# Performance work log

Measured on AMD Instinct MI355X. Metric: run time of the kernel, lower is better.

Reference implementation:

```python
import jax, jax.numpy as jnp
import numpy as np


def setup_inputs() -> dict:
    key = jax.random.key(0)
    ks = jax.random.split(key, 24)
    N, C, D_IN, HID, EMB = 8192, 4096, 32, 128, 128
    s = 0.05
    inp = {
        "cand_feat": jax.random.normal(ks[0], (1, C, D_IN), jnp.float32),
        "graph_pos": jax.random.uniform(ks[1], (N, 3), jnp.float32),
        "graph_rad": jax.random.uniform(ks[2], (N,), jnp.float32) + 0.01,
        "L": jnp.ones((1,), jnp.float32),
        "adj": jax.random.uniform(ks[3], (N, N), jnp.float32),
        "mask": jax.random.randint(ks[4], (1, C), 0, 2, jnp.int32),
        # candidate encoder: 32 -> 128 -> 128
        "cW1": jax.random.normal(ks[5], (D_IN, 128), jnp.float32) * s,
        "cb1": jnp.zeros((128,), jnp.float32),
        "cW2": jax.random.normal(ks[6], (128, EMB), jnp.float32) * s,
        "cb2": jnp.zeros((EMB,), jnp.float32),
        # graph encoder input proj: 4 -> 128
        "gW0": jax.random.normal(ks[7], (4, HID), jnp.float32) * s,
        "gb0": jnp.zeros((HID,), jnp.float32),
        # 3 GNN layers: concat(2*HID) -> HID
        "gnnW": jax.random.normal(ks[8], (3, 2 * HID, HID), jnp.float32) * s,
        "gnnb": jnp.zeros((3, HID), jnp.float32),
        # output proj: 2*HID -> EMB
        "goW": jax.random.normal(ks[9], (2 * HID, EMB), jnp.float32) * s,
        "gob": jnp.zeros((EMB,), jnp.float32),
        # fusion: 2*EMB -> 256 -> 128 -> 1
        "fW1": jax.random.normal(ks[10], (2 * EMB, 256), jnp.float32) * s,
        "fb1": jnp.zeros((256,), jnp.float32),
        "fW2": jax.random.normal(ks[11], (256, 128), jnp.float32) * s,
        "fb2": jnp.zeros((128,), jnp.float32),
        "fW3": jax.random.normal(ks[12], (128, 1), jnp.float32) * s,
        "fb3": jnp.zeros((1,), jnp.float32),
    }
    return inp


def reference(cand_feat, graph_pos, graph_rad, L, adj, mask,
              cW1, cb1, cW2, cb2, gW0, gb0, gnnW, gnnb, goW, gob,
              fW1, fb1, fW2, fb2, fW3, fb3):
    relu = jax.nn.relu
    # ---- candidate encoder: [1, C, 32] -> [1, C, 128]
    cand_emb = relu(relu(cand_feat @ cW1 + cb1) @ cW2 + cb2)
    # ---- graph encoder ----
    node = jnp.concatenate([graph_pos / L, (graph_rad / jnp.max(graph_rad))[:, None]], axis=1)  # [N, 4]
    h = relu(node @ gW0 + gb0)  # [N, HID]
    deg = jnp.clip(jnp.sum(adj, axis=-1, keepdims=True), 1.0)  # [N, 1]
    for i in range(gnnW.shape[0]):
        agg = (adj @ h) / deg                       # degree-normalized aggregation
        h = relu(jnp.concatenate([h, agg], axis=-1) @ gnnW[i] + gnnb[i])
    h_glob = jnp.concatenate([jnp.max(h, axis=0), jnp.mean(h, axis=0)], axis=-1)  # [2*HID]
    graph_emb = h_glob @ goW + gob  # [EMB]
    # ---- fusion decoder ----
    g_exp = jnp.broadcast_to(graph_emb[None, None, :], cand_emb.shape)
    combined = jnp.concatenate([cand_emb, g_exp], axis=-1)  # [1, C, 2*EMB]
    scores = (relu(relu(combined @ fW1 + fb1) @ fW2 + fb2) @ fW3 + fb3)[..., 0]  # [1, C]
    return jnp.where(mask == 0, -jnp.inf, scores)
```

## Files before the change

kernel.cpp:

```cpp
#include <hip/hip_runtime.h>
#include <hip/hip_bf16.h>

constexpr int NN  = 8192;
constexpr int CC  = 4096;
constexpr int HD  = 128;
constexpr int KSPLIT = 8;
constexpr int KCHUNK = NN / KSPLIT;
constexpr int NKB = KCHUNK / 32;
constexpr int NK32 = NN / 32;
constexpr int CCH = 32;

typedef __attribute__((ext_vector_type(8))) short bf16x8;
typedef __attribute__((ext_vector_type(4))) float f32x4;

static __device__ __forceinline__ unsigned short f2bf(float f) {
  unsigned int u = __builtin_bit_cast(unsigned int, f);
  unsigned int lsb = (u >> 16) & 1u;
  u += 0x7fffu + lsb;
  return (unsigned short)(u >> 16);
}
static __device__ __forceinline__ float bf2f(unsigned short u) {
  return __builtin_bit_cast(float, ((unsigned int)u) << 16);
}

static __device__ __forceinline__ size_t pidx(int t16, int kb, int lane) {
  return (((size_t)t16 * NK32 + kb) * 64 + lane) * 8;
}

__global__ __launch_bounds__(256) void k_radmax(const float* __restrict__ rad, float* out) {
  __shared__ float red[256];
  int t = threadIdx.x;
  float m = 0.0f;
  for (int i = t; i < NN; i += 256) m = fmaxf(m, rad[i]);
  red[t] = m; __syncthreads();
  for (int s = 128; s > 0; s >>= 1) {
    if (t < s) red[t] = fmaxf(red[t], red[t + s]);
    __syncthreads();
  }
  if (t == 0) out[0] = red[0];
}

__global__ __launch_bounds__(256) void k_h0(const float* __restrict__ pos, const float* __restrict__ rad,
                                            const float* __restrict__ Lp, const float* __restrict__ rmax,
                                            const float* __restrict__ gW0, const float* __restrict__ gb0,
                                            float* __restrict__ h, unsigned short* __restrict__ hTP) {
  __shared__ __align__(16) unsigned short lt[128][72];
  int t = threadIdx.x;
  int i0 = blockIdx.x * 64;
  float invL = 1.0f / Lp[0];
  float invR = 1.0f / rmax[0];
  for (int rep = 0; rep < 32; ++rep) {
    int idx = rep * 256 + t;
    int il = idx >> 7, j = idx & 127;
    int i = i0 + il;
    float n0 = pos[i * 3 + 0] * invL, n1 = pos[i * 3 + 1] * invL, n2 = pos[i * 3 + 2] * invL;
    float n3 = rad[i] * invR;
    float v = gb0[j] + n0 * gW0[j] + n1 * gW0[128 + j] + n2 * gW0[256 + j] + n3 * gW0[384 + j];
    v = fmaxf(v, 0.0f);
    h[(size_t)i * HD + j] = v;
    lt[j][il] = f2bf(v);
  }
  __syncthreads();
  #pragma unroll
  for (int it = 0; it < 4; ++it) {
    int idx = it * 256 + t;
    int lane = idx & 63, chunk = idx >> 6;
    int t16 = chunk >> 1, kbL = chunk & 1;
    int j = t16 * 16 + (lane & 15), kg = lane >> 4;
    union { unsigned short v[8]; uint4 q; } pk;
    #pragma unroll
    for (int s = 0; s < 8; ++s) {
      int kp = kg * 4 + (s & 3) + ((s >> 2) * 16);
      pk.v[s] = lt[j][kbL * 32 + kp];
    }
    *(uint4*)(hTP + pidx(t16, blockIdx.x * 2 + kbL, lane)) = pk.q;
  }
}

__global__ __launch_bounds__(256) void k_convP(const float* __restrict__ adj,
                                               unsigned short* __restrict__ adjP,
                                               float* __restrict__ pd) {
  __shared__ __align__(16) unsigned short lt[64 * 256];
  const int t = threadIdx.x;
  const int r0 = blockIdx.x * 64;
  const int c0 = blockIdx.y * 256;
  #pragma unroll
  for (int p = 0; p < 16; ++p) {
    int r = p * 4 + (t >> 6);
    int c = (t & 63) * 4;
    float4 v = *(const float4*)(adj + (size_t)(r0 + r) * NN + c0 + c);
    union { unsigned short u[4]; unsigned long long q; } pk;
    pk.u[0] = f2bf(v.x); pk.u[1] = f2bf(v.y); pk.u[2] = f2bf(v.z); pk.u[3] = f2bf(v.w);
    int g = c >> 3;
    int byte = r * 512 + (((g ^ (r & 7))) << 4) + ((c & 7) * 2);
    *(unsigned long long*)((char*)lt + byte) = pk.q;
  }
  __syncthreads();
  {
    int r = t >> 2, qd = t & 3;
    float s = 0.f;
    #pragma unroll
    for (int k4 = 0; k4 < 16; ++k4) {
      int kk = qd * 64 + k4 * 4;
      int byte = r * 512 + ((((kk >> 3) ^ (r & 7))) << 4) + ((kk & 7) * 2);
      union { unsigned long long q; unsigned short u[4]; } rd;
      rd.q = *(const unsigned long long*)((char*)lt + byte);
      s += bf2f(rd.u[0]) + bf2f(rd.u[1]) + bf2f(rd.u[2]) + bf2f(rd.u[3]);
    }
    s += __shfl_xor(s, 1);
    s += __shfl_xor(s, 2);
    if (qd == 0) pd[(size_t)blockIdx.y * NN + r0 + r] = s;
  }
  const int lane = t & 63, w = t >> 6;
  const int lr = lane & 15, kg = lane >> 4;
  #pragma unroll
  for (int it = 0; it < 8; ++it) {
    int chunk = it * 4 + w;
    int rtl = chunk >> 3, kbL = chunk & 7;
    int r = rtl * 16 + lr;
    union { unsigned short u[8]; uint4 q; } o;
    #pragma unroll
    for (int s = 0; s < 8; ++s) {
      int k = kbL * 32 + kg * 4 + (s & 3) + ((s >> 2) * 16);
      int byte = r * 512 + ((((k >> 3) ^ (r & 7))) << 4) + ((k & 7) * 2);
      o.u[s] = *(const unsigned short*)((char*)lt + byte);
    }
    *(uint4*)(adjP + pidx(blockIdx.x * 4 + rtl, (c0 >> 5) + kbL, lane)) = o.q;
  }
}

__global__ __launch_bounds__(256) void k_degsum(const float* __restrict__ pd, float* __restrict__ deg) {
  int i = blockIdx.x * 256 + threadIdx.x;
  float s = 0.f;
  #pragma unroll
  for (int c = 0; c < CCH; ++c) s += pd[(size_t)c * NN + i];
  deg[i] = fmaxf(s, 1.0f);
}

__global__ __launch_bounds__(256) void k_gemmP(const unsigned short* __restrict__ AP,
                                               const unsigned short* __restrict__ hTP,
                                               unsigned short* __restrict__ part) {
  __shared__ __align__(16) char smem[32768];
  const int t = threadIdx.x, lane = t & 63, w = t >> 6;
  const int bm = blockIdx.x, ks = blockIdx.y;
  const int kb0 = ks * NKB;
  const int lr = lane & 15, kg = lane >> 4;
  const int wr = w >> 1, wc = w & 1;

  const unsigned short* ap[4];
  const unsigned short* bp[4];
  #pragma unroll
  for (int q = 0; q < 4; ++q) {
    ap[q] = AP + pidx(bm * 8 + wr * 4 + q, kb0, lane);
    bp[q] = hTP + pidx(wc * 4 + q, kb0, lane);
  }

  f32x4 acc[4][4];
  #pragma unroll
  for (int i = 0; i < 4; ++i)
    #pragma unroll
    for (int j = 0; j < 4; ++j) acc[i][j] = f32x4{0.f, 0.f, 0.f, 0.f};

#define LDG_A(D, i_) { _Pragma("unroll") \
    for (int q = 0; q < 4; ++q) D[q] = *(const uint4*)(ap[q] + (size_t)(i_) * 512); }
#define LDG_B(D, i_) { _Pragma("unroll") \
    for (int q = 0; q < 4; ++q) D[q] = *(const uint4*)(bp[q] + (size_t)(i_) * 512); }
#define MM16(A_, B_) { _Pragma("unroll")                                  \
    for (int i = 0; i < 4; ++i) {                                         \
      union { uint4 q; bf16x8 v; } ua; ua.q = A_[i];                      \
      _Pragma("unroll")                                                   \
      for (int j = 0; j < 4; ++j) {                                       \
        union { uint4 q; bf16x8 v; } ub; ub.q = B_[j];                    \
        acc[i][j] = __builtin_amdgcn_mfma_f32_16x16x32_bf16(              \
            ua.v, ub.v, acc[i][j], 0, 0, 0);                              \
      } } }

  uint4 A0[4], B0[4], A1[4], B1[4];
  LDG_A(A0, 0); LDG_B(B0, 0);
  LDG_A(A1, 1); LDG_B(B1, 1);
  for (int kb = 0; kb + 3 < NKB; kb += 2) {
    MM16(A0, B0); LDG_A(A0, kb + 2); LDG_B(B0, kb + 2);
    MM16(A1, B1); LDG_A(A1, kb + 3); LDG_B(B1, kb + 3);
  }
  MM16(A0, B0);
  MM16(A1, B1);
#undef LDG_A
#undef LDG_B
#undef MM16

  __syncthreads();
  unsigned short* pl = (unsigned short*)smem;
  #pragma unroll
  for (int i = 0; i < 4; ++i)
    #pragma unroll
    for (int j = 0; j < 4; ++j)
      #pragma unroll
      for (int jj = 0; jj < 4; ++jj)
        pl[(wr * 64 + i * 16 + kg * 4 + jj) * 128 + wc * 64 + j * 16 + lr] =
            f2bf(acc[i][j][jj]);
  __syncthreads();
  uint4* gout = (uint4*)(part + (size_t)ks * NN * HD + (size_t)bm * 128 * HD);
  const uint4* ls = (const uint4*)smem;
  #pragma unroll
  for (int k = 0; k < 8; ++k) gout[k * 256 + t] = ls[k * 256 + t];
}

__global__ __launch_bounds__(256) void k_update(const unsigned short* __restrict__ part,
                                                const float* __restrict__ deg,
                                                const float* __restrict__ hin,
                                                const float* __restrict__ W, const float* __restrict__ bias,
                                                float* __restrict__ hout, unsigned short* __restrict__ hTP,
                                                int last) {
  __shared__ float cc[16][256];
  __shared__ __align__(16) unsigned short lt2[128][20];
  int t = threadIdx.x;
  int r0 = blockIdx.x * 16;
  for (int rep = 0; rep < 8; ++rep) {
    int idx = rep * 256 + t;
    int rl = idx >> 7, j = idx & 127;
    int row = r0 + rl;
    float s = 0.f;
    for (int ks = 0; ks < KSPLIT; ++ks)
      s += bf2f(part[((size_t)ks * NN + row) * HD + j]);
    cc[rl][128 + j] = s / deg[row];
    cc[rl][j] = hin[(size_t)row * HD + j];
  }
  __syncthreads();
  int jo = t & 127, rbase = t >> 7;
  float accv[8];
  float bj = bias[jo];
  for (int rr = 0; rr < 8; ++rr) accv[rr] = bj;
  for (int jj = 0; jj < 256; ++jj) {
    float wv = W[jj * HD + jo];
    for (int rr = 0; rr < 8; ++rr) accv[rr] += cc[rbase + rr * 2][jj] * wv;
  }
  for (int rr = 0; rr < 8; ++rr) {
    int rl = rbase + rr * 2;
    float v = fmaxf(accv[rr], 0.f);
    hout[(size_t)(r0 + rl) * HD + jo] = v;
    if (!last) lt2[jo][rl] = f2bf(v);
  }
  if (!last) {
    __syncthreads();
    const int p = (r0 >> 4) & 1;
    const int kb = r0 >> 5;
    #pragma unroll
    for (int it = 0; it < 2; ++it) {
      int idx = it * 256 + t;
      int lane = idx & 63, t16 = idx >> 6;
      int j = t16 * 16 + (lane & 15), kg = lane >> 4;
      union { unsigned short v[4]; uint2 q; } pk;
      #pragma unroll
      for (int d = 0; d < 4; ++d) pk.v[d] = lt2[j][kg * 4 + d];
      *(uint2*)(hTP + pidx(t16, kb, lane) + p * 4) = pk.q;
    }
  }
}

__global__ __launch_bounds__(256) void k_pool(const float* __restrict__ h,
                                              float* __restrict__ pmax, float* __restrict__ psum) {
  int b = blockIdx.x, t = threadIdx.x;
  int j = t & 127, half = t >> 7;
  int r0 = b * 128 + half * 64;
  float mx = -1e30f, sm = 0.f;
  for (int r = r0; r < r0 + 64; ++r) {
    float v = h[(size_t)r * HD + j];
    mx = fmaxf(mx, v); sm += v;
  }
  __shared__ float lm[2][128], ls[2][128];
  lm[half][j] = mx; ls[half][j] = sm;
  __syncthreads();
  if (half == 0) {
    pmax[b * 128 + j] = fmaxf(lm[0][j], lm[1][j]);
    psum[b * 128 + j] = ls[0][j] + ls[1][j];
  }
}

__global__ __launch_bounds__(256) void k_glob(const float* __restrict__ pmax, const float* __restrict__ psum,
                                              const float* __restrict__ goW, const float* __restrict__ gob,
                                              float* __restrict__ ge) {
  __shared__ float hg[256];
  int t = threadIdx.x;
  int j = t & 127, which = t >> 7;
  if (which == 0) {
    float m = -1e30f;
    for (int b = 0; b < 64; ++b) m = fmaxf(m, pmax[b * 128 + j]);
    hg[j] = m;
  } else {
    float s = 0.f;
    for (int b = 0; b < 64; ++b) s += psum[b * 128 + j];
    hg[128 + j] = s * (1.0f / (float)NN);
  }
  __syncthreads();
  if (t < 128) {
    float s = gob[t];
    for (int jj = 0; jj < 256; ++jj) s += hg[jj] * goW[jj * HD + t];
    ge[t] = s;
  }
}

__global__ __launch_bounds__(256) void k_fusion(const float* __restrict__ cand, const float* __restrict__ ge,
                                                const int* __restrict__ mask,
                                                const float* __restrict__ cW1, const float* __restrict__ cb1,
                                                const float* __restrict__ cW2, const float* __restrict__ cb2,
                                                const float* __restrict__ fW1, const float* __restrict__ fb1,
                                                const float* __restrict__ fW2, const float* __restrict__ fb2,
                                                const float* __restrict__ fW3, const float* __restrict__ fb3,
                                                float* __restrict__ out) {
  __shared__ float x[16][32];
  __shared__ float t1[16][128];
  __shared__ float t2[16][128];
  __shared__ float u1[16][256];
  __shared__ float u2[16][129];
  __shared__ float geL[128];
  int t = threadIdx.x;
  int c0 = blockIdx.x * 16;
  if (t < 128) geL[t] = ge[t];
  for (int rep = 0; rep < 2; ++rep) {
    int idx = rep * 256 + t;
    int cl = idx >> 5, d = idx & 31;
    x[cl][d] = cand[(size_t)(c0 + cl) * 32 + d];
  }
  __syncthreads();
  {
    int j = t & 127, cg = (t >> 7) * 8;
    float a[8]; float bj = cb1[j];
    for (int q = 0; q < 8; ++q) a[q] = bj;
    for (int d = 0; d < 32; ++d) {
      float wv = cW1[d * 128 + j];
      for (int q = 0; q < 8; ++q) a[q] += x[cg + q][d] * wv;
    }
    for (int q = 0; q < 8; ++q) t1[cg + q][j] = fmaxf(a[q], 0.f);
  }
  __syncthreads();
  {
    int j = t & 127, cg = (t >> 7) * 8;
    float a[8]; float bj = cb2[j];
    for (int q = 0; q < 8; ++q) a[q] = bj;
    for (int d = 0; d < 128; ++d) {
      float wv = cW2[d * 128 + j];
      for (int q = 0; q < 8; ++q) a[q] += t1[cg + q][d] * wv;
    }
    for (int q = 0; q < 8; ++q) t2[cg + q][j] = fmaxf(a[q], 0.f);
  }
  __syncthreads();
  {
    int jo = t;
    float gp = fb1[jo];
    for (int d = 0; d < 128; ++d) gp += geL[d] * fW1[(128 + d) * 256 + jo];
    float a[16];
    for (int q = 0; q < 16; ++q) a[q] = gp;
    for (int d = 0; d < 128; ++d) {
      float wv = fW1[d * 256 + jo];
      for (int q = 0; q < 16; ++q) a[q] += t2[q][d] * wv;
    }
    for (int q = 0; q < 16; ++q) u1[q][jo] = fmaxf(a[q], 0.f);
  }
  __syncthreads();
  {
    int j = t & 127, cg = (t >> 7) * 8;
    float a[8]; float bj = fb2[j];
    for (int q = 0; q < 8; ++q) a[q] = bj;
    for (int d = 0; d < 256; ++d) {
      float wv = fW2[d * 128 + j];
      for (int q = 0; q < 8; ++q) a[q] += u1[cg + q][d] * wv;
    }
    for (int q = 0; q < 8; ++q) u2[cg + q][j] = fmaxf(a[q], 0.f);
  }
  __syncthreads();
  if (t < 16) {
    int c = c0 + t;
    float s = fb3[0];
    for (int d = 0; d < 128; ++d) s += u2[t][d] * fW3[d];
    out[c] = (mask[c] == 0) ? -3.0e38f : s;
  }
}

extern "C" void kernel_launch(void* const* d_in, const int* in_sizes, int n_in,
                              void* d_out, int out_size, void* d_ws, size_t ws_size,
                              hipStream_t stream) {
  const float* cand = (const float*)d_in[0];
  const float* pos  = (const float*)d_in[1];
  const float* rad  = (const float*)d_in[2];
  const float* Lp   = (const float*)d_in[3];
  const float* adj  = (const float*)d_in[4];
  const int*   mask = (const int*)d_in[5];
  const float* cW1 = (const float*)d_in[6];
  const float* cb1 = (const float*)d_in[7];
  const float* cW2 = (const float*)d_in[8];
  const float* cb2 = (const float*)d_in[9];
  const float* gW0 = (const float*)d_in[10];
  const float* gb0 = (const float*)d_in[11];
  const float* gnnW = (const float*)d_in[12];
  const float* gnnb = (const float*)d_in[13];
  const float* goW = (const float*)d_in[14];
  const float* gob = (const float*)d_in[15];
  const float* fW1 = (const float*)d_in[16];
  const float* fb1 = (const float*)d_in[17];
  const float* fW2 = (const float*)d_in[18];
  const float* fb2 = (const float*)d_in[19];
  const float* fW3 = (const float*)d_in[20];
  const float* fb3 = (const float*)d_in[21];

  char* ws = (char*)d_ws;
  float* h            = (float*)ws;
  unsigned short* hTP = (unsigned short*)(ws + (4ull << 20));
  float* rmax         = (float*)(ws + (6ull << 20));
  float* pmax         = (float*)(ws + (6ull << 20) + 4096);
  float* psum         = pmax + 64 * 128;
  float* ge           = psum + 64 * 128;
  float* deg          = (float*)(ws + (6ull << 20) + (128u << 10));
  float* pd           = (float*)(ws + (7ull << 20));
  unsigned short* part = (unsigned short*)(ws + (8ull << 20));
  unsigned short* adjP = (unsigned short*)(ws + (25ull << 20));

  k_radmax<<<1, 256, 0, stream>>>(rad, rmax);
  k_h0<<<NN / 64, 256, 0, stream>>>(pos, rad, Lp, rmax, gW0, gb0, h, hTP);
  {
    dim3 gc(NN / 64, CCH);
    k_convP<<<gc, 256, 0, stream>>>(adj, adjP, pd);
  }
  k_degsum<<<NN / 256, 256, 0, stream>>>(pd, deg);

  dim3 g(NN / 128, KSPLIT);
  for (int l = 0; l < 3; ++l) {
    k_gemmP<<<g, 256, 0, stream>>>(adjP, hTP, part);
    k_update<<<NN / 16, 256, 0, stream>>>(part, deg, h,
                                          gnnW + l * 256 * HD, gnnb + l * HD, h, hTP, l == 2);
  }
  k_pool<<<64, 256, 0, stream>>>(h, pmax, psum);
  k_glob<<<1, 256, 0, stream>>>(pmax, psum, goW, gob, ge);
  k_fusion<<<CC / 16, 256, 0, stream>>>(cand, ge, mask, cW1, cb1, cW2, cb2,
                                        fW1, fb1, fW2, fb2, fW3, fb3, (float*)d_out);
}
```

Measured before the change: 403.1 us.

## Fuse adjacency bf16 conversion and degree sum into first aggregation GEMM

Drops the separate adjacency conversion and degree-sum kernels. The first GNN-layer GEMM now reads the fp32 adjacency directly, converts it to bf16 in registers, writes the packed bf16 copy for later layers, and accumulates per-row partial degrees, which k_update then reduces. It also deepens the register prefetch in k_gemmP from 2 to 4 stages. If the workspace is too small, every layer falls back to re-reading fp32 adj. The costs are a first GEMM with no prefetch pipeline and degrees now summed in fp32 instead of from bf16-rounded values.

```diff
diff --git a/kernel.cpp b/kernel.cpp
--- a/kernel.cpp
+++ b/kernel.cpp
@@ -8,7 +8,6 @@
 constexpr int KCHUNK = NN / KSPLIT;
 constexpr int NKB = KCHUNK / 32;
 constexpr int NK32 = NN / 32;
-constexpr int CCH = 32;
 
 typedef __attribute__((ext_vector_type(8))) short bf16x8;
 typedef __attribute__((ext_vector_type(4))) float f32x4;
@@ -77,64 +76,94 @@
   }
 }
 
-__global__ __launch_bounds__(256) void k_convP(const float* __restrict__ adj,
-                                               unsigned short* __restrict__ adjP,
-                                               float* __restrict__ pd) {
-  __shared__ __align__(16) unsigned short lt[64 * 256];
-  const int t = threadIdx.x;
-  const int r0 = blockIdx.x * 64;
-  const int c0 = blockIdx.y * 256;
+#define MM16(A_, B_) { _Pragma("unroll")                                  \
+    for (int i = 0; i < 4; ++i) {                                         \
+      union { uint4 q; bf16x8 v; } ua; ua.q = A_[i];                      \
+      _Pragma("unroll")                                                   \
+      for (int j = 0; j < 4; ++j) {                                       \
+        union { uint4 q; bf16x8 v; } ub; ub.q = B_[j];                    \
+        acc[i][j] = __builtin_amdgcn_mfma_f32_16x16x32_bf16(              \
+            ua.v, ub.v, acc[i][j], 0, 0, 0);                              \
+      } } }
+
+#define EPILOGUE128(smem_, dst_)                                          \
+  do {                                                                    \
+    __syncthreads();                                                      \
+    unsigned short* pl = (unsigned short*)(smem_);                        \
+    _Pragma("unroll")                                                     \
+    for (int i = 0; i < 4; ++i)                                           \
+      _Pragma("unroll")                                                   \
+      for (int j = 0; j < 4; ++j)                                         \
+        _Pragma("unroll")                                                 \
+        for (int jj = 0; jj < 4; ++jj)                                    \
+          pl[(wr * 64 + i * 16 + kg * 4 + jj) * 128 + wc * 64 + j * 16 + lr] = \
+              f2bf(acc[i][j][jj]);                                        \
+    __syncthreads();                                                      \
+    uint4* gout = (uint4*)(dst_);                                         \
+    const uint4* ls = (const uint4*)(smem_);                              \
+    _Pragma("unroll")                                                     \
+    for (int k = 0; k < 8; ++k) gout[k * 256 + t] = ls[k * 256 + t];      \
+  } while (0)
+
+template <int WB>
+__global__ __launch_bounds__(256) void k_gemm1P(const float* __restrict__ A32,
+                                                const unsigned short* __restrict__ hTP,
+                                                unsigned short* __restrict__ adjP,
+                                                float* __restrict__ part_deg,
+                                                unsigned short* __restrict__ part) {
+  __shared__ __align__(16) char smem[32768];
+  const int t = threadIdx.x, lane = t & 63, w = t >> 6;
+  const int bm = blockIdx.x, ks = blockIdx.y;
+  const int kb0 = ks * NKB;
+  const int lr = lane & 15, kg = lane >> 4;
+  const int wr = w >> 1, wc = w & 1;
+
+  const float* ap32[4];
+  unsigned short* apk[4];
+  const unsigned short* bp[4];
   #pragma unroll
-  for (int p = 0; p < 16; ++p) {
-    int r = p * 4 + (t >> 6);
-    int c = (t & 63) * 4;
-    float4 v = *(const float4*)(adj + (size_t)(r0 + r) * NN + c0 + c);
-    union { unsigned short u[4]; unsigned long long q; } pk;
-    pk.u[0] = f2bf(v.x); pk.u[1] = f2bf(v.y); pk.u[2] = f2bf(v.z); pk.u[3] = f2bf(v.w);
-    int g = c >> 3;
-    int byte = r * 512 + (((g ^ (r & 7))) << 4) + ((c & 7) * 2);
-    *(unsigned long long*)((char*)lt + byte) = pk.q;
-  }
-  __syncthreads();
-  {
-    int r = t >> 2, qd = t & 3;
-    float s = 0.f;
-    #pragma unroll
-    for (int k4 = 0; k4 < 16; ++k4) {
-      int kk = qd * 64 + k4 * 4;
-      int byte = r * 512 + ((((kk >> 3) ^ (r & 7))) << 4) + ((kk & 7) * 2);
-      union { unsigned long long q; unsigned short u[4]; } rd;
-      rd.q = *(const unsigned long long*)((char*)lt + byte);
-      s += bf2f(rd.u[0]) + bf2f(rd.u[1]) + bf2f(rd.u[2]) + bf2f(rd.u[3]);
-    }
-    s += __shfl_xor(s, 1);
-    s += __shfl_xor(s, 2);
-    if (qd == 0) pd[(size_t)blockIdx.y * NN + r0 + r] = s;
-  }
-  const int lane = t & 63, w = t >> 6;
-  const int lr = lane & 15, kg = lane >> 4;
+  for (int q = 0; q < 4; ++q) {
+    ap32[q] = A32 + (size_t)(bm * 128 + wr * 64 + q * 16 + lr) * NN + (size_t)kb0 * 32 + kg * 4;
+    if (WB) apk[q] = adjP + pidx(bm * 8 + wr * 4 + q, kb0, lane);
+    bp[q] = hTP + pidx(wc * 4 + q, kb0, lane);
+  }
+
+  f32x4 acc[4][4];
   #pragma unroll
-  for (int it = 0; it < 8; ++it) {
-    int chunk = it * 4 + w;
-    int rtl = chunk >> 3, kbL = chunk & 7;
-    int r = rtl * 16 + lr;
-    union { unsigned short u[8]; uint4 q; } o;
-    #pragma unroll
-    for (int s = 0; s < 8; ++s) {
-      int k = kbL * 32 + kg * 4 + (s & 3) + ((s >> 2) * 16);
-      int byte = r * 512 + ((((k >> 3) ^ (r & 7))) << 4) + ((k & 7) * 2);
-      o.u[s] = *(const unsigned short*)((char*)lt + byte);
-    }
-    *(uint4*)(adjP + pidx(blockIdx.x * 4 + rtl, (c0 >> 5) + kbL, lane)) = o.q;
-  }
-}
-
-__global__ __launch_bounds__(256) void k_degsum(const float* __restrict__ pd, float* __restrict__ deg) {
-  int i = blockIdx.x * 256 + threadIdx.x;
-  float s = 0.f;
-  #pragma unroll
-  for (int c = 0; c < CCH; ++c) s += pd[(size_t)c * NN + i];
-  deg[i] = fmaxf(s, 1.0f);
+  for (int i = 0; i < 4; ++i)
+    #pragma unroll
+    for (int j = 0; j < 4; ++j) acc[i][j] = f32x4{0.f, 0.f, 0.f, 0.f};
+  float rs[4] = {0.f, 0.f, 0.f, 0.f};
+
+  for (int kb = 0; kb < NKB; ++kb) {
+    uint4 Af[4], Bf[4];
+    #pragma unroll
+    for (int q = 0; q < 4; ++q) {
+      float4 lo = *(const float4*)(ap32[q] + kb * 32);
+      float4 hi = *(const float4*)(ap32[q] + kb * 32 + 16);
+      union { unsigned short u[8]; uint4 qq; } pk;
+      pk.u[0] = f2bf(lo.x); pk.u[1] = f2bf(lo.y); pk.u[2] = f2bf(lo.z); pk.u[3] = f2bf(lo.w);
+      pk.u[4] = f2bf(hi.x); pk.u[5] = f2bf(hi.y); pk.u[6] = f2bf(hi.z); pk.u[7] = f2bf(hi.w);
+      Af[q] = pk.qq;
+      rs[q] += lo.x + lo.y + lo.z + lo.w + hi.x + hi.y + hi.z + hi.w;
+      if (WB && wc == 0) *(uint4*)(apk[q] + (size_t)kb * 512) = pk.qq;
+      Bf[q] = *(const uint4*)(bp[q] + (size_t)kb * 512);
+    }
+    MM16(Af, Bf);
+  }
+
+  if (wc == 0) {
+    #pragma unroll
+    for (int q = 0; q < 4; ++q) {
+      float v = rs[q];
+      v += __shfl_xor(v, 16);
+      v += __shfl_xor(v, 32);
+      if (kg == 0)
+        part_deg[(size_t)ks * NN + bm * 128 + wr * 64 + q * 16 + lr] = v;
+    }
+  }
+
+  EPILOGUE128(smem, part + (size_t)ks * NN * HD + (size_t)bm * 128 * HD);
 }
 
 __global__ __launch_bounds__(256) void k_gemmP(const unsigned short* __restrict__ AP,
@@ -165,56 +194,45 @@
     for (int q = 0; q < 4; ++q) D[q] = *(const uint4*)(ap[q] + (size_t)(i_) * 512); }
 #define LDG_B(D, i_) { _Pragma("unroll") \
     for (int q = 0; q < 4; ++q) D[q] = *(const uint4*)(bp[q] + (size_t)(i_) * 512); }
-#define MM16(A_, B_) { _Pragma("unroll")                                  \
-    for (int i = 0; i < 4; ++i) {                                         \
-      union { uint4 q; bf16x8 v; } ua; ua.q = A_[i];                      \
-      _Pragma("unroll")                                                   \
-      for (int j = 0; j < 4; ++j) {                                       \
-        union { uint4 q; bf16x8 v; } ub; ub.q = B_[j];                    \
-        acc[i][j] = __builtin_amdgcn_mfma_f32_16x16x32_bf16(              \
-            ua.v, ub.v, acc[i][j], 0, 0, 0);                              \
-      } } }
-
-  uint4 A0[4], B0[4], A1[4], B1[4];
+
+  uint4 A0[4], A1[4], A2[4], A3[4], B0[4], B1[4], B2[4], B3[4];
   LDG_A(A0, 0); LDG_B(B0, 0);
   LDG_A(A1, 1); LDG_B(B1, 1);
-  for (int kb = 0; kb + 3 < NKB; kb += 2) {
-    MM16(A0, B0); LDG_A(A0, kb + 2); LDG_B(B0, kb + 2);
-    MM16(A1, B1); LDG_A(A1, kb + 3); LDG_B(B1, kb + 3);
+  LDG_A(A2, 2); LDG_B(B2, 2);
+  LDG_A(A3, 3); LDG_B(B3, 3);
+  for (int kb = 0; kb + 7 < NKB; kb += 4) {
+    MM16(A0, B0); LDG_A(A0, kb + 4); LDG_B(B0, kb + 4);
+    MM16(A1, B1); LDG_A(A1, kb + 5); LDG_B(B1, kb + 5);
+    MM16(A2, B2); LDG_A(A2, kb + 6); LDG_B(B2, kb + 6);
+    MM16(A3, B3); LDG_A(A3, kb + 7); LDG_B(B3, kb + 7);
   }
   MM16(A0, B0);
   MM16(A1, B1);
+  MM16(A2, B2);
+  MM16(A3, B3);
 #undef LDG_A
 #undef LDG_B
-#undef MM16
-
-  __syncthreads();
-  unsigned short* pl = (unsigned short*)smem;
-  #pragma unroll
-  for (int i = 0; i < 4; ++i)
-    #pragma unroll
-    for (int j = 0; j < 4; ++j)
-      #pragma unroll
-      for (int jj = 0; jj < 4; ++jj)
-        pl[(wr * 64 + i * 16 + kg * 4 + jj) * 128 + wc * 64 + j * 16 + lr] =
-            f2bf(acc[i][j][jj]);
-  __syncthreads();
-  uint4* gout = (uint4*)(part + (size_t)ks * NN * HD + (size_t)bm * 128 * HD);
-  const uint4* ls = (const uint4*)smem;
-  #pragma unroll
-  for (int k = 0; k < 8; ++k) gout[k * 256 + t] = ls[k * 256 + t];
+
+  EPILOGUE128(smem, part + (size_t)ks * NN * HD + (size_t)bm * 128 * HD);
 }
 
 __global__ __launch_bounds__(256) void k_update(const unsigned short* __restrict__ part,
-                                                const float* __restrict__ deg,
+                                                const float* __restrict__ part_deg,
                                                 const float* __restrict__ hin,
                                                 const float* __restrict__ W, const float* __restrict__ bias,
                                                 float* __restrict__ hout, unsigned short* __restrict__ hTP,
                                                 int last) {
   __shared__ float cc[16][256];
+  __shared__ float degS[16];
   __shared__ __align__(16) unsigned short lt2[128][20];
   int t = threadIdx.x;
   int r0 = blockIdx.x * 16;
+  if (t < 16) {
+    float d = 0.f;
+    for (int ks = 0; ks < KSPLIT; ++ks) d += part_deg[(size_t)ks * NN + r0 + t];
+    degS[t] = fmaxf(d, 1.0f);
+  }
+  __syncthreads();
   for (int rep = 0; rep < 8; ++rep) {
     int idx = rep * 256 + t;
     int rl = idx >> 7, j = idx & 127;
@@ -222,7 +240,7 @@
     float s = 0.f;
     for (int ks = 0; ks < KSPLIT; ++ks)
       s += bf2f(part[((size_t)ks * NN + row) * HD + j]);
-    cc[rl][128 + j] = s / deg[row];
+    cc[rl][128 + j] = s / degS[rl];
     cc[rl][j] = hin[(size_t)row * HD + j];
   }
   __syncthreads();
@@ -409,23 +427,25 @@
   float* pmax         = (float*)(ws + (6ull << 20) + 4096);
   float* psum         = pmax + 64 * 128;
   float* ge           = psum + 64 * 128;
-  float* deg          = (float*)(ws + (6ull << 20) + (128u << 10));
-  float* pd           = (float*)(ws + (7ull << 20));
+  float* part_deg     = (float*)(ws + (7ull << 20));
   unsigned short* part = (unsigned short*)(ws + (8ull << 20));
   unsigned short* adjP = (unsigned short*)(ws + (25ull << 20));
 
+  bool big = ws_size >= (25ull << 20) + (size_t)NN * NN * 2;
+
   k_radmax<<<1, 256, 0, stream>>>(rad, rmax);
   k_h0<<<NN / 64, 256, 0, stream>>>(pos, rad, Lp, rmax, gW0, gb0, h, hTP);
-  {
-    dim3 gc(NN / 64, CCH);
-    k_convP<<<gc, 256, 0, stream>>>(adj, adjP, pd);
-  }
-  k_degsum<<<NN / 256, 256, 0, stream>>>(pd, deg);
 
   dim3 g(NN / 128, KSPLIT);
   for (int l = 0; l < 3; ++l) {
-    k_gemmP<<<g, 256, 0, stream>>>(adjP, hTP, part);
-    k_update<<<NN / 16, 256, 0, stream>>>(part, deg, h,
+    if (l == 0) {
+      if (big) k_gemm1P<1><<<g, 256, 0, stream>>>(adj, hTP, adjP, part_deg, part);
+      else     k_gemm1P<0><<<g, 256, 0, stream>>>(adj, hTP, nullptr, part_deg, part);
+    } else {
+      if (big) k_gemmP<<<g, 256, 0, stream>>>(adjP, hTP, part);
+      else     k_gemm1P<0><<<g, 256, 0, stream>>>(adj, hTP, nullptr, part_deg, part);
+    }
+    k_update<<<NN / 16, 256, 0, stream>>>(part, part_deg, h,
                                           gnnW + l * 256 * HD, gnnb + l * HD, h, hTP, l == 2);
   }
   k_pool<<<64, 256, 0, stream>>>(h, pmax, psum);
```

After: 427.4 us. 6.0% more time.

## Triple-buffer GEMM global loads with inline asm and scalar base addresses

Applied to the files above, without the earlier changes.

Rewrites the k_gemmP main loop as a three-stage register pipeline. Global loads are issued through inline asm global_load_dwordx4 using a scalar (readfirstlane) base plus a lane voffset, and explicit vmcnt waits and sched_barriers keep two k-blocks in flight while the MFMAs consume the third. The aim is to hide global memory latency better and cut per-lane address arithmetic. In exchange it uses more VGPRs for the extra stage, hardcodes the loop trip count (10x3+2 = 32 k-blocks, matching NKB), and relies on the manual waitcnt counts being right.

```diff
diff --git a/kernel.cpp b/kernel.cpp
--- a/kernel.cpp
+++ b/kernel.cpp
@@ -21,6 +21,11 @@
 }
 static __device__ __forceinline__ float bf2f(unsigned short u) {
   return __builtin_bit_cast(float, ((unsigned int)u) << 16);
+}
+static __device__ __forceinline__ unsigned long long rfl64(unsigned long long x) {
+  unsigned int lo = __builtin_amdgcn_readfirstlane((unsigned int)x);
+  unsigned int hi = __builtin_amdgcn_readfirstlane((unsigned int)(x >> 32));
+  return ((unsigned long long)hi << 32) | lo;
 }
 
 static __device__ __forceinline__ size_t pidx(int t16, int kb, int lane) {
@@ -137,6 +142,22 @@
   deg[i] = fmaxf(s, 1.0f);
 }
 
+#define MM16(A_, B_) { _Pragma("unroll")                                  \
+    for (int i = 0; i < 4; ++i) {                                         \
+      union { uint4 q; bf16x8 v; } ua; ua.q = A_[i];                      \
+      _Pragma("unroll")                                                   \
+      for (int j = 0; j < 4; ++j) {                                       \
+        union { uint4 q; bf16x8 v; } ub; ub.q = B_[j];                    \
+        acc[i][j] = __builtin_amdgcn_mfma_f32_16x16x32_bf16(              \
+            ua.v, ub.v, acc[i][j], 0, 0, 0);                              \
+      } } }
+
+#define GLD(dst, base, imm)                                               \
+  asm volatile("global_load_dwordx4 %0, %1, %2 offset:" #imm              \
+               : "=v"(dst) : "v"(voff), "s"(base))
+#define WAITV(n) do { asm volatile("s_waitcnt vmcnt(" #n ")");            \
+                      __builtin_amdgcn_sched_barrier(0); } while (0)
+
 __global__ __launch_bounds__(256) void k_gemmP(const unsigned short* __restrict__ AP,
                                                const unsigned short* __restrict__ hTP,
                                                unsigned short* __restrict__ part) {
@@ -146,13 +167,13 @@
   const int kb0 = ks * NKB;
   const int lr = lane & 15, kg = lane >> 4;
   const int wr = w >> 1, wc = w & 1;
-
-  const unsigned short* ap[4];
-  const unsigned short* bp[4];
+  const unsigned int voff = (unsigned int)(lane * 16);
+
+  unsigned long long bA[4], bB[4];
   #pragma unroll
   for (int q = 0; q < 4; ++q) {
-    ap[q] = AP + pidx(bm * 8 + wr * 4 + q, kb0, lane);
-    bp[q] = hTP + pidx(wc * 4 + q, kb0, lane);
+    bA[q] = rfl64((unsigned long long)(AP + pidx(bm * 8 + wr * 4 + q, kb0, 0)));
+    bB[q] = rfl64((unsigned long long)(hTP + pidx(wc * 4 + q, kb0, 0)));
   }
 
   f32x4 acc[4][4];
@@ -161,32 +182,36 @@
     #pragma unroll
     for (int j = 0; j < 4; ++j) acc[i][j] = f32x4{0.f, 0.f, 0.f, 0.f};
 
-#define LDG_A(D, i_) { _Pragma("unroll") \
-    for (int q = 0; q < 4; ++q) D[q] = *(const uint4*)(ap[q] + (size_t)(i_) * 512); }
-#define LDG_B(D, i_) { _Pragma("unroll") \
-    for (int q = 0; q < 4; ++q) D[q] = *(const uint4*)(bp[q] + (size_t)(i_) * 512); }
-#define MM16(A_, B_) { _Pragma("unroll")                                  \
-    for (int i = 0; i < 4; ++i) {                                         \
-      union { uint4 q; bf16x8 v; } ua; ua.q = A_[i];                      \
-      _Pragma("unroll")                                                   \
-      for (int j = 0; j < 4; ++j) {                                       \
-        union { uint4 q; bf16x8 v; } ub; ub.q = B_[j];                    \
-        acc[i][j] = __builtin_amdgcn_mfma_f32_16x16x32_bf16(              \
-            ua.v, ub.v, acc[i][j], 0, 0, 0);                              \
-      } } }
-
-  uint4 A0[4], B0[4], A1[4], B1[4];
-  LDG_A(A0, 0); LDG_B(B0, 0);
-  LDG_A(A1, 1); LDG_B(B1, 1);
-  for (int kb = 0; kb + 3 < NKB; kb += 2) {
-    MM16(A0, B0); LDG_A(A0, kb + 2); LDG_B(B0, kb + 2);
-    MM16(A1, B1); LDG_A(A1, kb + 3); LDG_B(B1, kb + 3);
-  }
-  MM16(A0, B0);
-  MM16(A1, B1);
-#undef LDG_A
-#undef LDG_B
-#undef MM16
+  uint4 S0a[4], S0b[4], S1a[4], S1b[4], S2a[4], S2b[4];
+
+  #pragma unroll
+  for (int q = 0; q < 4; ++q) { GLD(S0a[q], bA[q], 0); GLD(S0b[q], bB[q], 0); }
+  #pragma unroll
+  for (int q = 0; q < 4; ++q) { GLD(S1a[q], bA[q], 1024); GLD(S1b[q], bB[q], 1024); }
+
+#define PHASE(CA, CB, NA, NB)                                             \
+  do {                                                                    \
+    _Pragma("unroll")                                                     \
+    for (int q = 0; q < 4; ++q) { GLD(NA[q], bA[q], 2048);                \
+                                  GLD(NB[q], bB[q], 2048); }              \
+    _Pragma("unroll")                                                     \
+    for (int q = 0; q < 4; ++q) { bA[q] += 1024; bB[q] += 1024; }         \
+    WAITV(16);                                                            \
+    MM16(CA, CB);                                                         \
+    __builtin_amdgcn_sched_barrier(0);                                    \
+  } while (0)
+
+  for (int r = 0; r < 10; ++r) {
+    PHASE(S0a, S0b, S2a, S2b);
+    PHASE(S1a, S1b, S0a, S0b);
+    PHASE(S2a, S2b, S1a, S1b);
+  }
+  WAITV(8);
+  MM16(S0a, S0b);
+  __builtin_amdgcn_sched_barrier(0);
+  WAITV(0);
+  MM16(S1a, S1b);
+#undef PHASE
 
   __syncthreads();
   unsigned short* pl = (unsigned short*)smem;
```

Result: no change. 401.0 us (-0.5%).
